# Performance work log

Measured on AMD Instinct MI355X. Metric: run time of the kernel, lower is better.

Reference implementation:

```python
import jax, jax.numpy as jnp
import numpy as np

NUM_TAGS = 64
SOS_IDX, EOS_IDX, PAD_IDX = 1, 2, 0
NEG = -10000.0


def _make_trans(key):
    t = np.array(jax.random.normal(key, (NUM_TAGS, NUM_TAGS), dtype=jnp.float32))
    t[SOS_IDX, :] = NEG
    t[:, EOS_IDX] = NEG
    t[:, PAD_IDX] = NEG
    t[PAD_IDX, :] = NEG
    t[PAD_IDX, EOS_IDX] = 0.0
    t[PAD_IDX, PAD_IDX] = 0.0
    return jnp.asarray(t)


def setup_inputs() -> dict:
    key = jax.random.key(0)
    k_h, k_len, k_tr = jax.random.split(key, 3)
    B, T = 256, 1024
    h = jax.random.normal(k_h, (B, T, NUM_TAGS), dtype=jnp.float32)
    # variable-length prefix mask (1.0 for valid steps)
    lengths = jax.random.randint(k_len, (B,), 1, T + 1)
    mask = (jnp.arange(T)[None, :] < lengths[:, None]).astype(jnp.float32)
    trans = _make_trans(k_tr)
    return {"h": h, "mask": mask, "trans": trans}


def reference(h, mask, trans):
    # h: [B, T, N] emissions; mask: [B, T]; trans: [N_next, N_prev]
    B, T, N = h.shape
    init = jnp.full((B, N), NEG, dtype=h.dtype).at[:, SOS_IDX].set(0.0)

    def step(score, xs):
        h_t, m_t = xs  # [B, N], [B]
        # score[b, prev] + emit[b, next] + trans[next, prev] -> lse over prev
        s = score[:, None, :] + h_t[:, :, None] + trans[None, :, :]
        new = jax.nn.logsumexp(s, axis=-1)  # [B, N]
        m = m_t[:, None]
        score = new * m + score * (1.0 - m)
        return score, None

    score, _ = jax.lax.scan(step, init, (jnp.swapaxes(h, 0, 1), mask.T))
    # terminal transition to EOS, then partition function per batch element
    return jax.nn.logsumexp(score + trans[EOS_IDX][None, :], axis=-1)  # [B]
```

## Files before the change

kernel.cpp:

```cpp
#include <hip/hip_runtime.h>

#define BATCH 256
#define TT 1024
#define NN 64
#define CHUNK 64
#define NCH 16
#define SOS 1
#define EOSI 2
#define LN2F 0.6931471805599453f
#define LOG2E 1.4426950408889634f

typedef short bf16x8 __attribute__((ext_vector_type(8)));
typedef float f32x4 __attribute__((ext_vector_type(4)));

__device__ __forceinline__ unsigned short f2bf(float x) {
  unsigned u = __float_as_uint(x);
  u += 0x7fffu + ((u >> 16) & 1u);
  return (unsigned short)(u >> 16);
}
__device__ __forceinline__ float bf2f(unsigned short v) { return __uint_as_float(((unsigned)v) << 16); }
__device__ __forceinline__ unsigned cvtpk(float lo, float hi) {
  unsigned r;
  asm("v_cvt_pk_bf16_f32 %0, %1, %2" : "=v"(r) : "v"(lo), "v"(hi));
  return r;
}

__device__ __forceinline__ int padr(int k, int c) {
  return ((k >> 5) << 10) + (((k >> 3) & 3) << 8) + (c << 4) + ((k & 7) << 1);
}

__device__ __forceinline__ int wave_len(const float* mask, int b, int l) {
  float ls = 0.f;
#pragma unroll
  for (int c = 0; c < 4; ++c) {
    float4 m4 = *reinterpret_cast<const float4*>(mask + (size_t)b * TT + c * 256 + l * 4);
    ls += (m4.x + m4.y) + (m4.z + m4.w);
  }
#pragma unroll
  for (int m = 1; m < 64; m <<= 1) ls += __shfl_xor(ls, m, 64);
  return (int)(ls + 0.5f);
}

__global__ __launch_bounds__(256, 4) void crf_chunk(const float* __restrict__ h,
                                                    const float* __restrict__ mask,
                                                    const float* __restrict__ trans,
                                                    unsigned short* __restrict__ mats,
                                                    int* __restrict__ scalesI) {
  __shared__ char lds[4 * 2048 + 4 * 512];
  const int tid = threadIdx.x;
  const int w = tid >> 6;
  const int l = tid & 63;
  const int h4 = l >> 4;
  const int cl = l & 15;
  char* P = lds + w * 2048;
  float* ehs0 = (float*)(lds + 8192 + w * 512);
  float* ehs1 = ehs0 + 64;

  const int b = blockIdx.x & (BATCH - 1);
  const int c = blockIdx.x >> 8;

  const int len = wave_len(mask, b, l);
  const int t0 = c * CHUNK;
  if (t0 >= len) return;
  const int nstep = min(CHUNK, len - t0);

  bf16x8 ef[4][2];
#pragma unroll
  for (int I = 0; I < 4; ++I)
#pragma unroll
    for (int Kc = 0; Kc < 2; ++Kc) {
      const float* p = trans + (16 * I + cl) * 64 + 32 * Kc + 8 * h4;
      bf16x8 v;
#pragma unroll
      for (int e = 0; e < 8; ++e) v[e] = (short)f2bf(__expf(p[e]));
      ef[I][Kc] = v;
    }

#pragma unroll
  for (int i = 0; i < 2; ++i) *(f32x4*)(P + ((i * 64 + l) << 4)) = f32x4{0.f, 0.f, 0.f, 0.f};
  if (l < 16) *(unsigned short*)(P + padr(16 * w + l, l)) = 0x3F80;

  const float* hb = h + ((size_t)b * TT + t0) * NN + l;
  ehs0[l] = exp2f(hb[0] * LOG2E);
  asm volatile("" ::: "memory");

  float hvN = hb[(size_t)min(1, nstep - 1) * NN];
  float hvN2 = hb[(size_t)min(2, nstep - 1) * NN];
  int esum = 0, ecCur = 0, eM1 = 0;

  for (int t = 0; t < nstep; ++t) {
    esum += ecCur;
    float* ehsW = ((t + 1) & 1) ? ehs1 : ehs0;
    ehsW[l] = exp2f(fmaf(hvN, LOG2E, -(float)eM1));
    ecCur = eM1;
    hvN = hvN2;
    hvN2 = hb[(size_t)min(t + 3, nstep - 1) * NN];

    float* ehsR = (t & 1) ? ehs1 : ehs0;
    bf16x8 fc0 = *(bf16x8*)(P + (l << 4));
    bf16x8 fc1 = *(bf16x8*)(P + 1024 + (l << 4));
    f32x4 eh4[4];
#pragma unroll
    for (int I = 0; I < 4; ++I) eh4[I] = *(f32x4*)(ehsR + 16 * I + 4 * h4);

    f32x4 a[4];
#pragma unroll
    for (int I = 0; I < 4; ++I) a[I] = f32x4{0.f, 0.f, 0.f, 0.f};
#pragma unroll
    for (int I = 0; I < 4; ++I) {
      a[I] = __builtin_amdgcn_mfma_f32_16x16x32_bf16(ef[I][0], fc0, a[I], 0, 0, 0);
      a[I] = __builtin_amdgcn_mfma_f32_16x16x32_bf16(ef[I][1], fc1, a[I], 0, 0, 0);
    }
    float prox = 0.f;
#pragma unroll
    for (int I = 0; I < 4; ++I) {
      f32x4 v = a[I] * eh4[I];
      prox = fmaxf(prox, fmaxf(fmaxf(v[0], v[1]), fmaxf(v[2], v[3])));
      *(uint2*)(P + padr(16 * I + 4 * h4, cl)) = uint2{cvtpk(v[0], v[1]), cvtpk(v[2], v[3])};
    }
    prox = fmaxf(prox, __shfl_xor(prox, 16, 64));
    prox = fmaxf(prox, __shfl_xor(prox, 32, 64));
    float px = __int_as_float(__builtin_amdgcn_readlane(__float_as_int(prox), 5));
    eM1 = (__float_as_int(px) >> 23) - 127;
    asm volatile("" ::: "memory");
  }

  const float scF = __int_as_float((127 - eM1) << 23);
  esum += eM1;
  unsigned short* gm = mats + (size_t)(b * NCH + c) * 4096 + l * 64 + 16 * w;
  unsigned q[8];
#pragma unroll
  for (int p = 0; p < 8; ++p) {
    float x0 = bf2f(*(unsigned short*)(P + padr(l, 2 * p))) * scF;
    float x1 = bf2f(*(unsigned short*)(P + padr(l, 2 * p + 1))) * scF;
    q[p] = cvtpk(x0, x1);
  }
  *(uint4*)gm = uint4{q[0], q[1], q[2], q[3]};
  *(uint4*)(gm + 8) = uint4{q[4], q[5], q[6], q[7]};
  if (l == 0) scalesI[(b * NCH + c) * 4 + w] = esum;
}

__global__ __launch_bounds__(64) void crf_fold(const float* __restrict__ mask,
                                               const float* __restrict__ trans,
                                               const unsigned short* __restrict__ mats,
                                               const int* __restrict__ scalesI,
                                               float* __restrict__ out) {
  __shared__ float pv[NN];
  const int l = threadIdx.x;
  const int b = blockIdx.x;
  const int len = wave_len(mask, b, l);
  const int nc = (len + CHUNK - 1) / CHUNK;

  float pr = (l == SOS) ? 1.f : 0.f;
  int eA = 0;
  long esumT = 0;

  for (int c = 0; c < nc; ++c) {
    const int* sI = scalesI + (b * NCH + c) * 4;
    const int e0 = sI[0], e1 = sI[1], e2 = sI[2], e3 = sI[3];
    const int S = max(max(e0, e1), max(e2, e3));
    const int g = l >> 4;
    int dl = (g == 0) ? e0 : (g == 1) ? e1 : (g == 2) ? e2 : e3;
    dl -= S;
    pv[l] = ldexpf(pr, dl - eA);
    asm volatile("" ::: "memory");
    esumT += S + eA;

    const uint4* Mr = (const uint4*)(mats + (size_t)(b * NCH + c) * 4096 + l * 64);
    uint4 U[8];
#pragma unroll
    for (int j = 0; j < 8; ++j) U[j] = Mr[j];
    float ac0 = 0.f, ac1 = 0.f, ac2 = 0.f, ac3 = 0.f;
#pragma unroll
    for (int j = 0; j < 8; ++j) {
      f32x4 pa = *(f32x4*)(pv + j * 8);
      f32x4 pb = *(f32x4*)(pv + j * 8 + 4);
      uint4 qq = U[j];
      ac0 = fmaf(__uint_as_float(qq.x << 16), pa[0], ac0);
      ac1 = fmaf(__uint_as_float(qq.x & 0xffff0000u), pa[1], ac1);
      ac2 = fmaf(__uint_as_float(qq.y << 16), pa[2], ac2);
      ac3 = fmaf(__uint_as_float(qq.y & 0xffff0000u), pa[3], ac3);
      ac0 = fmaf(__uint_as_float(qq.z << 16), pb[0], ac0);
      ac1 = fmaf(__uint_as_float(qq.z & 0xffff0000u), pb[1], ac1);
      ac2 = fmaf(__uint_as_float(qq.w << 16), pb[2], ac2);
      ac3 = fmaf(__uint_as_float(qq.w & 0xffff0000u), pb[3], ac3);
    }
    pr = (ac0 + ac1) + (ac2 + ac3);
    float mm = pr;
#pragma unroll
    for (int m = 1; m < 64; m <<= 1) mm = fmaxf(mm, __shfl_xor(mm, m, 64));
    eA = (__float_as_int(mm) >> 23) - 127;
    asm volatile("" ::: "memory");
  }

  float s = pr * __expf(trans[EOSI * NN + l]);
#pragma unroll
  for (int m = 1; m < 64; m <<= 1) s += __shfl_xor(s, m, 64);
  if (l == 0) out[b] = __logf(s) + LN2F * (float)esumT;
}

extern "C" void kernel_launch(void* const* d_in, const int* in_sizes, int n_in,
                              void* d_out, int out_size, void* d_ws, size_t ws_size,
                              hipStream_t stream) {
  const float* h = (const float*)d_in[0];
  const float* mask = (const float*)d_in[1];
  const float* trans = (const float*)d_in[2];
  float* out = (float*)d_out;

  unsigned short* mats = (unsigned short*)d_ws;
  int* scalesI = (int*)((char*)d_ws + (size_t)BATCH * NCH * 4096 * 2);

  hipLaunchKernelGGL(crf_chunk, dim3(BATCH * NCH), dim3(256), 0, stream, h, mask, trans, mats, scalesI);
  hipLaunchKernelGGL(crf_fold, dim3(BATCH), dim3(64), 0, stream, mask, trans, mats, scalesI, out);
}
```

Measured before the change: 154.7 us.

## Prefetch bf16 emission factors a step ahead and renormalize every four steps

Emission exponentials are now stored as bf16 in a double-buffered LDS slot and loaded one step early, so the serial recurrence no longer waits on the LDS read of the current emissions. The max-reduction with shuffle and readlane that picks the rescale exponent now runs only every fourth step, and its result is folded into a later emission. This takes the cross-lane reduction off most iterations of the loop. Block indexing changes so that consecutive blocks cover the chunks of one batch element, which spreads variable sequence lengths differently across the GPU. The cost is lower emission precision and a wider dynamic range between rescales.

```diff
diff --git a/kernel.cpp b/kernel.cpp
--- a/kernel.cpp
+++ b/kernel.cpp
@@ -46,18 +46,16 @@
                                                     const float* __restrict__ trans,
                                                     unsigned short* __restrict__ mats,
                                                     int* __restrict__ scalesI) {
-  __shared__ char lds[4 * 2048 + 4 * 512];
+  __shared__ __align__(16) char lds[4 * 2048 + 4 * 256];
   const int tid = threadIdx.x;
-  const int w = tid >> 6;
-  const int l = tid & 63;
-  const int h4 = l >> 4;
-  const int cl = l & 15;
+  const int w = tid >> 6, l = tid & 63;
+  const int h4 = l >> 4, cl = l & 15;
+  const int b = blockIdx.x >> 4;
+  const int c = blockIdx.x & (NCH - 1);
+
   char* P = lds + w * 2048;
-  float* ehs0 = (float*)(lds + 8192 + w * 512);
-  float* ehs1 = ehs0 + 64;
-
-  const int b = blockIdx.x & (BATCH - 1);
-  const int c = blockIdx.x >> 8;
+  char* ehB = lds + 8192 + w * 256;
+  const int wp = 2 * (16 * ((l >> 2) & 3) + 4 * (l >> 4) + (l & 3));
 
   const int len = wave_len(mask, b, l);
   const int t0 = c * CHUNK;
@@ -81,28 +79,29 @@
   if (l < 16) *(unsigned short*)(P + padr(16 * w + l, l)) = 0x3F80;
 
   const float* hb = h + ((size_t)b * TT + t0) * NN + l;
-  ehs0[l] = exp2f(hb[0] * LOG2E);
-  asm volatile("" ::: "memory");
-
+  *(unsigned short*)(ehB + wp) = f2bf(exp2f(hb[0] * LOG2E));
+  uint4 ua = *(uint4*)(ehB + 32 * h4);
+  uint4 ub = *(uint4*)(ehB + 32 * h4 + 16);
   float hvN = hb[(size_t)min(1, nstep - 1) * NN];
   float hvN2 = hb[(size_t)min(2, nstep - 1) * NN];
-  int esum = 0, ecCur = 0, eM1 = 0;
+  asm volatile("" ::: "memory");
+
+  int esum = 0, ePend = 0;
+  int pp = 128;
+  uint4 uaN = ua, ubN = ub;
 
   for (int t = 0; t < nstep; ++t) {
-    esum += ecCur;
-    float* ehsW = ((t + 1) & 1) ? ehs1 : ehs0;
-    ehsW[l] = exp2f(fmaf(hvN, LOG2E, -(float)eM1));
-    ecCur = eM1;
-    hvN = hvN2;
-    hvN2 = hb[(size_t)min(t + 3, nstep - 1) * NN];
-
-    float* ehsR = (t & 1) ? ehs1 : ehs0;
+    if (t + 1 < nstep) {
+      const int ec = (((t + 1) & 3) == 0) ? ePend : 0;
+      esum += ec;
+      *(unsigned short*)(ehB + pp + wp) = f2bf(exp2f(fmaf(hvN, LOG2E, (float)(-ec))));
+      uaN = *(uint4*)(ehB + pp + 32 * h4);
+      ubN = *(uint4*)(ehB + pp + 32 * h4 + 16);
+      hvN = hvN2;
+      hvN2 = hb[(size_t)min(t + 3, nstep - 1) * NN];
+    }
     bf16x8 fc0 = *(bf16x8*)(P + (l << 4));
     bf16x8 fc1 = *(bf16x8*)(P + 1024 + (l << 4));
-    f32x4 eh4[4];
-#pragma unroll
-    for (int I = 0; I < 4; ++I) eh4[I] = *(f32x4*)(ehsR + 16 * I + 4 * h4);
-
     f32x4 a[4];
 #pragma unroll
     for (int I = 0; I < 4; ++I) a[I] = f32x4{0.f, 0.f, 0.f, 0.f};
@@ -111,22 +110,32 @@
       a[I] = __builtin_amdgcn_mfma_f32_16x16x32_bf16(ef[I][0], fc0, a[I], 0, 0, 0);
       a[I] = __builtin_amdgcn_mfma_f32_16x16x32_bf16(ef[I][1], fc1, a[I], 0, 0, 0);
     }
+    const bool meas = ((t & 3) == 2);
     float prox = 0.f;
 #pragma unroll
     for (int I = 0; I < 4; ++I) {
-      f32x4 v = a[I] * eh4[I];
-      prox = fmaxf(prox, fmaxf(fmaxf(v[0], v[1]), fmaxf(v[2], v[3])));
+      const unsigned d0 = (I == 0) ? ua.x : (I == 1) ? ua.z : (I == 2) ? ub.x : ub.z;
+      const unsigned d1 = (I == 0) ? ua.y : (I == 1) ? ua.w : (I == 2) ? ub.y : ub.w;
+      f32x4 eh = {__uint_as_float(d0 << 16), __uint_as_float(d0 & 0xffff0000u),
+                  __uint_as_float(d1 << 16), __uint_as_float(d1 & 0xffff0000u)};
+      f32x4 v = a[I] * eh;
+      if (meas) prox = fmaxf(prox, fmaxf(fmaxf(v[0], v[1]), fmaxf(v[2], v[3])));
       *(uint2*)(P + padr(16 * I + 4 * h4, cl)) = uint2{cvtpk(v[0], v[1]), cvtpk(v[2], v[3])};
     }
-    prox = fmaxf(prox, __shfl_xor(prox, 16, 64));
-    prox = fmaxf(prox, __shfl_xor(prox, 32, 64));
-    float px = __int_as_float(__builtin_amdgcn_readlane(__float_as_int(prox), 5));
-    eM1 = (__float_as_int(px) >> 23) - 127;
+    if (meas) {
+      prox = fmaxf(prox, __shfl_xor(prox, 16, 64));
+      prox = fmaxf(prox, __shfl_xor(prox, 32, 64));
+      const float px = __int_as_float(__builtin_amdgcn_readlane(__float_as_int(prox), 5));
+      ePend = (__float_as_int(px) >> 23) - 127;
+    }
+    ua = uaN;
+    ub = ubN;
+    pp ^= 128;
     asm volatile("" ::: "memory");
   }
 
-  const float scF = __int_as_float((127 - eM1) << 23);
-  esum += eM1;
+  const float scF = __int_as_float((127 - ePend) << 23);
+  esum += ePend;
   unsigned short* gm = mats + (size_t)(b * NCH + c) * 4096 + l * 64 + 16 * w;
   unsigned q[8];
 #pragma unroll
```

After: 225.2 us. 1.46x slower.
